# Performance work log

Hardware: AMD Instinct MI355X
Metric: run time of the kernel (lower is better)

## Reference

```python
import math
import jax, jax.numpy as jnp
import numpy as np

B, T, D, H, FACTOR = 8, 4096, 1024, 16, 5
DH = D // H


def setup_inputs() -> dict:
    key = jax.random.key(0)
    ks = jax.random.split(key, 7)
    u = max(1, min(int(FACTOR * math.log(T + 1)), T))  # = 41
    s = 1.0 / np.sqrt(D).astype(np.float32)
    x = jax.random.normal(ks[0], (B, T, D), jnp.float32)
    Wq = jax.random.normal(ks[1], (D, D), jnp.float32) * s
    Wk = jax.random.normal(ks[2], (D, D), jnp.float32) * s
    Wv = jax.random.normal(ks[3], (D, D), jnp.float32) * s
    Wo = jax.random.normal(ks[4], (D, D), jnp.float32) * s
    bo = jax.random.normal(ks[5], (D,), jnp.float32) * 0.01
    # unique indices, mirroring torch.randperm(T)[:u]
    idx = jax.random.permutation(ks[6], T)[:u].astype(jnp.int32)
    return {"x": x, "Wq": Wq, "Wk": Wk, "Wv": Wv, "Wo": Wo, "bo": bo, "idx": idx}


def reference(x, Wq, Wk, Wv, Wo, bo, idx):
    Bx, Tx, Dx = x.shape
    scale = 1.0 / np.sqrt(DH).astype(np.float32)

    def proj(W):  # torch Linear: x @ W.T, then split heads -> [B,H,T,Dh]
        return (x @ W.T).reshape(Bx, Tx, H, DH).transpose(0, 2, 1, 3)

    Q = proj(Wq)
    K = proj(Wk)
    V = proj(Wv)

    Qs = Q[:, :, idx, :]                                   # [B,H,u,Dh] gather
    scores = jnp.einsum('bhud,bhtd->bhut', Qs, K) * scale  # [B,H,u,T]
    attn = jax.nn.softmax(scores, axis=-1)
    ctx = jnp.einsum('bhut,bhtd->bhud', attn, V)           # [B,H,u,Dh]

    # mean over the u sampled positions fills non-sampled slots
    out = jnp.broadcast_to(ctx.mean(axis=2, keepdims=True), (Bx, H, Tx, DH))
    out = out.at[:, :, idx, :].set(ctx)                    # scatter ctx back

    y = out.transpose(0, 2, 1, 3).reshape(Bx, Tx, Dx)
    return y @ Wo.T + bo
```

## Files before the change

### kernel.cpp

```cpp
#include <hip/hip_runtime.h>
#include <hip/hip_bf16.h>

#define B_  8
#define T_  4096
#define D_  1024
#define H_  16
#define DH_ 64
#define NC_ 4

typedef __bf16 bf8 __attribute__((ext_vector_type(8)));
typedef float f32x4 __attribute__((ext_vector_type(4)));

__device__ __forceinline__ unsigned short f2bf_rn(float f) {
    unsigned u = __float_as_uint(f);
    unsigned r = (u + 0x7FFF + ((u >> 16) & 1)) >> 16;
    return (unsigned short)r;
}

__device__ __forceinline__ void async_load16(const void* gp, void* lp) {
    __builtin_amdgcn_global_load_lds(
        (const __attribute__((address_space(1))) unsigned*)(gp),
        (__attribute__((address_space(3))) unsigned*)(lp), 16, 0, 0);
}


__global__ void k_sel(const int* __restrict__ idx, int* __restrict__ sel, int U) {
    for (int t = threadIdx.x; t < T_; t += 256) sel[t] = 0;
    __syncthreads();
    if (threadIdx.x < U) sel[idx[threadIdx.x]] = threadIdx.x + 1;
}

__global__ void k_gather(const float* __restrict__ x, const int* __restrict__ idx,
                         float* __restrict__ xs, int U) {
    int bi = blockIdx.x;
    int b = bi / U, i = bi - b * U;
    int t = idx[i];
    const float4* src = (const float4*)(x + ((size_t)(b * T_ + t)) * D_);
    float4* dst = (float4*)(xs + (size_t)bi * D_);
    dst[threadIdx.x] = src[threadIdx.x];
}

__global__ void k_cvt_flat(const float* __restrict__ src, short* __restrict__ dst) {
    size_t i = ((size_t)blockIdx.x * 256 + threadIdx.x) * 8;
    float4 a = *(const float4*)(src + i);
    float4 b = *(const float4*)(src + i + 4);
    short4 s0, s1;
    s0.x = (short)f2bf_rn(a.x); s0.y = (short)f2bf_rn(a.y);
    s0.z = (short)f2bf_rn(a.z); s0.w = (short)f2bf_rn(a.w);
    s1.x = (short)f2bf_rn(b.x); s1.y = (short)f2bf_rn(b.y);
    s1.z = (short)f2bf_rn(b.z); s1.w = (short)f2bf_rn(b.w);
    *(short4*)(dst + i) = s0;
    *(short4*)(dst + i + 4) = s1;
}

__global__ void k_zpad(short* __restrict__ Qtb, int HU, int MP) {
    int bi = blockIdx.x;
    int npad = MP - HU;
    int b = bi / npad, r = bi - b * npad;
    short4 z = {0, 0, 0, 0};
    *(short4*)(Qtb + ((size_t)b * MP + HU + r) * D_ + threadIdx.x * 4) = z;
}

__global__ __launch_bounds__(256) void k_proj(const float* __restrict__ A,
                                              const float* __restrict__ W,
                                              const float* __restrict__ bias,
                                              float* __restrict__ C, int M) {
    __shared__ float As[32][64 + 4];
    __shared__ float Bs[32][64 + 4];
    int m0 = blockIdx.x * 64, n0 = blockIdx.y * 64;
    int tid = threadIdx.x;
    int lr = tid >> 3;
    int lc = (tid & 7) * 4;
    int ty = tid >> 4, tx = tid & 15;
    float acc[4][4] = {{0.f}};
    for (int k0 = 0; k0 < D_; k0 += 32) {
#pragma unroll
        for (int half = 0; half < 2; ++half) {
            int r = lr + half * 32;
            int gm = m0 + r;
            float4 v = make_float4(0.f, 0.f, 0.f, 0.f);
            if (gm < M) v = *(const float4*)(A + (size_t)gm * D_ + k0 + lc);
            As[lc + 0][r] = v.x; As[lc + 1][r] = v.y; As[lc + 2][r] = v.z; As[lc + 3][r] = v.w;
            int gn = n0 + r;
            float4 w = *(const float4*)(W + (size_t)gn * D_ + k0 + lc);
            Bs[lc + 0][r] = w.x; Bs[lc + 1][r] = w.y; Bs[lc + 2][r] = w.z; Bs[lc + 3][r] = w.w;
        }
        __syncthreads();
#pragma unroll
        for (int kk = 0; kk < 32; ++kk) {
            float4 a = *(const float4*)&As[kk][ty * 4];
            float4 bb = *(const float4*)&Bs[kk][tx * 4];
            acc[0][0] += a.x * bb.x; acc[0][1] += a.x * bb.y; acc[0][2] += a.x * bb.z; acc[0][3] += a.x * bb.w;
            acc[1][0] += a.y * bb.x; acc[1][1] += a.y * bb.y; acc[1][2] += a.y * bb.z; acc[1][3] += a.y * bb.w;
            acc[2][0] += a.z * bb.x; acc[2][1] += a.z * bb.y; acc[2][2] += a.z * bb.z; acc[2][3] += a.z * bb.w;
            acc[3][0] += a.w * bb.x; acc[3][1] += a.w * bb.y; acc[3][2] += a.w * bb.z; acc[3][3] += a.w * bb.w;
        }
        __syncthreads();
    }
#pragma unroll
    for (int i = 0; i < 4; ++i) {
        int gm = m0 + ty * 4 + i;
        if (gm < M) {
            int gn = n0 + tx * 4;
            float4 v = make_float4(acc[i][0], acc[i][1], acc[i][2], acc[i][3]);
            if (bias) {
                v.x += bias[gn + 0]; v.y += bias[gn + 1];
                v.z += bias[gn + 2]; v.w += bias[gn + 3];
            }
            *(float4*)(C + (size_t)gm * D_ + gn) = v;
        }
    }
}

__global__ __launch_bounds__(256) void k_qth(const float* __restrict__ Qs,
                                             const float* __restrict__ Wk,
                                             short* __restrict__ Qtb, int U, int MP) {
    __shared__ float As[32][64 + 4];
    __shared__ float Bs[32][64 + 4];
    int h = blockIdx.z;
    int m0 = blockIdx.x * 64, n0 = blockIdx.y * 64;
    int BU = B_ * U;
    int tid = threadIdx.x;
    int lr = tid >> 3, lc = (tid & 7) * 4;
    int ty = tid >> 4, tx = tid & 15;
    float acc[4][4] = {{0.f}};
    for (int k0 = 0; k0 < DH_; k0 += 32) {
#pragma unroll
        for (int half = 0; half < 2; ++half) {
            int r = lr + half * 32;
            int gm = m0 + r;
            float4 v = make_float4(0.f, 0.f, 0.f, 0.f);
            if (gm < BU) v = *(const float4*)(Qs + (size_t)gm * D_ + h * DH_ + k0 + lc);
            As[lc + 0][r] = v.x; As[lc + 1][r] = v.y; As[lc + 2][r] = v.z; As[lc + 3][r] = v.w;
            int kr = (tid >> 4) + half * 16;
            int nc = (tid & 15) * 4;
            float4 w = *(const float4*)(Wk + ((size_t)(h * DH_ + k0 + kr)) * D_ + n0 + nc);
            *(float4*)&Bs[kr][nc] = w;
        }
        __syncthreads();
#pragma unroll
        for (int kk = 0; kk < 32; ++kk) {
            float4 a = *(const float4*)&As[kk][ty * 4];
            float4 bb = *(const float4*)&Bs[kk][tx * 4];
            acc[0][0] += a.x * bb.x; acc[0][1] += a.x * bb.y; acc[0][2] += a.x * bb.z; acc[0][3] += a.x * bb.w;
            acc[1][0] += a.y * bb.x; acc[1][1] += a.y * bb.y; acc[1][2] += a.y * bb.z; acc[1][3] += a.y * bb.w;
            acc[2][0] += a.z * bb.x; acc[2][1] += a.z * bb.y; acc[2][2] += a.z * bb.z; acc[2][3] += a.z * bb.w;
            acc[3][0] += a.w * bb.x; acc[3][1] += a.w * bb.y; acc[3][2] += a.w * bb.z; acc[3][3] += a.w * bb.w;
        }
        __syncthreads();
    }
#pragma unroll
    for (int i = 0; i < 4; ++i) {
        int gm = m0 + ty * 4 + i;
        if (gm < BU) {
            int b = gm / U, ii = gm - b * U;
            short4 s;
            s.x = (short)f2bf_rn(0.125f * acc[i][0]);
            s.y = (short)f2bf_rn(0.125f * acc[i][1]);
            s.z = (short)f2bf_rn(0.125f * acc[i][2]);
            s.w = (short)f2bf_rn(0.125f * acc[i][3]);
            *(short4*)(Qtb + ((size_t)b * MP + h * U + ii) * D_ + n0 + tx * 4) = s;
        }
    }
}

__global__ __launch_bounds__(256) void k_scores_exp(const short* __restrict__ A,
                                                    const short* __restrict__ Bt,
                                                    short* __restrict__ attnb, int MP) {
    __shared__ short As[128 * 32];
    __shared__ short Bs[128 * 32];
    int g = blockIdx.x;
    int n8 = (g >> 3) & 3;
    int m = (g >> 5) % 6;
    int b = (g >> 5) / 6;
    int n = (g & 7) + 8 * n8;
    const int K = D_;
    const short* Ab = A + (size_t)b * MP * K;
    const short* Bb = Bt + (size_t)b * T_ * K;
    short* Cb = attnb + (size_t)b * MP * T_;
    int m0 = m * 128, n0 = n * 128;
    int tid = threadIdx.x;
    int lane = tid & 63, w = tid >> 6;
    int wr = w >> 1, wc = w & 1;

    f32x4 acc[4][4];
#pragma unroll
    for (int mi = 0; mi < 4; ++mi)
#pragma unroll
        for (int ni = 0; ni < 4; ++ni)
            acc[mi][ni] = (f32x4){0.f, 0.f, 0.f, 0.f};

    int arow = wr * 64 + (lane & 15);
    int brow = wc * 64 + (lane & 15);
    int koff = (lane >> 4) * 8;

    for (int kt = 0; kt < K; kt += 32) {
#pragma unroll
        for (int i = 0; i < 2; ++i) {
            int li = i * 256 + tid;
            int row = li >> 2, kc = (li & 3) << 3;
            async_load16(Ab + (size_t)(m0 + row) * K + kt + kc, As + li * 8);
            async_load16(Bb + (size_t)(n0 + row) * K + kt + kc, Bs + li * 8);
        }
        __syncthreads();
        bf8 af[4], bfr[4];
#pragma unroll
        for (int mi = 0; mi < 4; ++mi)
            af[mi] = *(const bf8*)(As + (arow + mi * 16) * 32 + koff);
#pragma unroll
        for (int ni = 0; ni < 4; ++ni)
            bfr[ni] = *(const bf8*)(Bs + (brow + ni * 16) * 32 + koff);
#pragma unroll
        for (int mi = 0; mi < 4; ++mi)
#pragma unroll
            for (int ni = 0; ni < 4; ++ni)
                acc[mi][ni] = __builtin_amdgcn_mfma_f32_16x16x32_bf16(af[mi], bfr[ni], acc[mi][ni], 0, 0, 0);
        __syncthreads();
    }

    int cr = (lane >> 4) * 4, cc = lane & 15;
#pragma unroll
    for (int mi = 0; mi < 4; ++mi)
#pragma unroll
        for (int ni = 0; ni < 4; ++ni) {
            int col = n0 + wc * 64 + ni * 16 + cc;
#pragma unroll
            for (int r = 0; r < 4; ++r) {
                float e = __expf(acc[mi][ni][r]);
                int grow = m0 + wr * 64 + mi * 16 + cr + r;
                Cb[(size_t)grow * T_ + col] = (short)f2bf_rn(e);
            }
        }
}

__global__ __launch_bounds__(256) void k_v(const short* __restrict__ xb,
                                           const short* __restrict__ Wvb,
                                           short* __restrict__ Vt) {
    __shared__ short smem[8192];
    short* As = smem;
    short* Bs = smem + 4096;
    int g = blockIdx.x;
    int mr = g & 7, n = (g >> 3) & 7, mq = g >> 6;
    int m = mq * 8 + mr;
    const int K = D_;
    const short* Ab = xb + (size_t)m * 128 * K;
    const short* Bb = Wvb + (size_t)n * 128 * K;
    int tid = threadIdx.x;
    int lane = tid & 63, w = tid >> 6;
    int wr = w >> 1, wc = w & 1;

    f32x4 acc[4][4];
#pragma unroll
    for (int mi = 0; mi < 4; ++mi)
#pragma unroll
        for (int ni = 0; ni < 4; ++ni)
            acc[mi][ni] = (f32x4){0.f, 0.f, 0.f, 0.f};

    int arow = wr * 64 + (lane & 15);
    int brow = wc * 64 + (lane & 15);
    int koff = (lane >> 4) * 8;

    for (int kt = 0; kt < K; kt += 32) {
#pragma unroll
        for (int i = 0; i < 2; ++i) {
            int li = i * 256 + tid;
            int row = li >> 2, kc = (li & 3) << 3;
            async_load16(Ab + (size_t)row * K + kt + kc, As + li * 8);
            async_load16(Bb + (size_t)row * K + kt + kc, Bs + li * 8);
        }
        __syncthreads();
        bf8 af[4], bfr[4];
#pragma unroll
        for (int mi = 0; mi < 4; ++mi)
            af[mi] = *(const bf8*)(As + (arow + mi * 16) * 32 + koff);
#pragma unroll
        for (int ni = 0; ni < 4; ++ni)
            bfr[ni] = *(const bf8*)(Bs + (brow + ni * 16) * 32 + koff);
#pragma unroll
        for (int mi = 0; mi < 4; ++mi)
#pragma unroll
            for (int ni = 0; ni < 4; ++ni)
                acc[mi][ni] = __builtin_amdgcn_mfma_f32_16x16x32_bf16(af[mi], bfr[ni], acc[mi][ni], 0, 0, 0);
        __syncthreads();
    }

    int b = m >> 5;
    int tG0 = (m & 31) * 128 + wr * 64;
    int h = n * 2 + wc;
    short* ep = smem + w * 2048;
    const int PITCH = 72;
    int quad = lane >> 4;
#pragma unroll
    for (int ni = 0; ni < 4; ++ni) {
#pragma unroll
        for (int mi = 0; mi < 4; ++mi) {
            int t = mi * 16 + quad * 4;
            int dh = lane & 15;
#pragma unroll
            for (int r = 0; r < 4; ++r)
                ep[dh * PITCH + t + r] = (short)f2bf_rn(acc[mi][ni][r]);
        }
        __syncthreads();
#pragma unroll
        for (int it = 0; it < 2; ++it) {
            int dhl = it * 8 + (lane >> 3);
            int seg = lane & 7;
            bf8 v = *(const bf8*)(ep + dhl * PITCH + seg * 8);
            int dh = ni * 16 + dhl;
            *(bf8*)(Vt + ((size_t)(b * H_ + h) * DH_ + dh) * T_ + tG0 + seg * 8) = v;
        }
        __syncthreads();
    }
}

__global__ __launch_bounds__(256) void k_pv(const short* __restrict__ attnb,
                                            const short* __restrict__ Vt,
                                            float* __restrict__ Op,
                                            float* __restrict__ rsp,
                                            int U, int MP) {
    __shared__ short vt[64 * 136];
    int gid = blockIdx.x;
    int c = gid & (NC_ - 1);
    int bh = gid >> 2;
    int h = bh & (H_ - 1);
    int b = bh >> 4;
    int tid = threadIdx.x;
    int lane = tid & 63, w = tid >> 6;
    int quad = lane >> 4;
    const short* Arow = attnb + ((size_t)b * MP + h * U) * T_;
    const short* Vrow = Vt + (size_t)bh * DH_ * T_;

    f32x4 O[3];
#pragma unroll
    for (int mi = 0; mi < 3; ++mi) O[mi] = (f32x4){0.f, 0.f, 0.f, 0.f};
    float rs[3] = {0.f, 0.f, 0.f};

    for (int tt = 0; tt < (T_ / NC_) / 128; ++tt) {
        int t0 = c * (T_ / NC_) + tt * 128;
#pragma unroll
        for (int it = 0; it < 4; ++it) {
            int idx = it * 256 + tid;
            int dh = idx >> 4, seg = idx & 15;
            bf8 v = *(const bf8*)(Vrow + (size_t)dh * T_ + t0 + seg * 8);
            *(bf8*)(vt + dh * 136 + seg * 8) = v;
        }
        __syncthreads();
        bf8 af[3][4];
#pragma unroll
        for (int mi = 0; mi < 3; ++mi)
#pragma unroll
            for (int kf = 0; kf < 4; ++kf)
                af[mi][kf] = *(const bf8*)(Arow + (size_t)(mi * 16 + (lane & 15)) * T_ + t0 + kf * 32 + quad * 8);
        if (w == 0) {
#pragma unroll
            for (int mi = 0; mi < 3; ++mi)
#pragma unroll
                for (int kf = 0; kf < 4; ++kf)
#pragma unroll
                    for (int j = 0; j < 8; ++j) rs[mi] += (float)af[mi][kf][j];
        }
#pragma unroll
        for (int kf = 0; kf < 4; ++kf) {
            bf8 bfr = *(const bf8*)(vt + (w * 16 + (lane & 15)) * 136 + kf * 32 + quad * 8);
#pragma unroll
            for (int mi = 0; mi < 3; ++mi)
                O[mi] = __builtin_amdgcn_mfma_f32_16x16x32_bf16(af[mi][kf], bfr, O[mi], 0, 0, 0);
        }
        __syncthreads();
    }
#pragma unroll
    for (int mi = 0; mi < 3; ++mi)
#pragma unroll
        for (int r = 0; r < 4; ++r)
            Op[((size_t)gid * 48 + mi * 16 + quad * 4 + r) * DH_ + w * 16 + (lane & 15)] = O[mi][r];
    if (w == 0) {
#pragma unroll
        for (int mi = 0; mi < 3; ++mi) {
            rs[mi] += __shfl_xor(rs[mi], 16);
            rs[mi] += __shfl_xor(rs[mi], 32);
            if (quad == 0) rsp[(size_t)gid * 48 + mi * 16 + lane] = rs[mi];
        }
    }
}

__global__ __launch_bounds__(256) void k_rows2(const float* __restrict__ Op,
                                               const float* __restrict__ rsp,
                                               float* __restrict__ R, int U) {
    __shared__ float inv[48];
    __shared__ float msum[4][64];
    int bh = blockIdx.x;
    int b = bh >> 4, h = bh & (H_ - 1);
    int tid = threadIdx.x;
    if (tid < 48) {
        float s = 0.f;
        for (int cc = 0; cc < NC_; ++cc) s += rsp[(size_t)(bh * NC_ + cc) * 48 + tid];
        inv[tid] = 1.f / s;
    }
    __syncthreads();
    int dh = tid & 63, ig = tid >> 6;
    float acc = 0.f;
    for (int p = 0; p < 11; ++p) {
        int i = p * 4 + ig;
        if (i < U) {
            float o = 0.f;
            for (int cc = 0; cc < NC_; ++cc)
                o += Op[((size_t)(bh * NC_ + cc) * 48 + i) * DH_ + dh];
            float v = o * inv[i];
            R[((size_t)b * (U + 1) + 1 + i) * D_ + h * DH_ + dh] = v;
            acc += v;
        }
    }
    msum[ig][dh] = acc;
    __syncthreads();
    if (ig == 0)
        R[((size_t)b * (U + 1)) * D_ + h * DH_ + dh] =
            (msum[0][dh] + msum[1][dh] + msum[2][dh] + msum[3][dh]) / (float)U;
}

__global__ __launch_bounds__(256) void k_fill(const float* __restrict__ Yr,
                                              const int* __restrict__ sel,
                                              float* __restrict__ y, int U) {
    int blk = blockIdx.x;
    int b = blk >> 12, t = blk & (T_ - 1);
    int j = sel[t];
    const float4* src = (const float4*)(Yr + ((size_t)b * (U + 1) + j) * D_);
    float4* dst = (float4*)(y + (size_t)blk * D_);
    dst[threadIdx.x] = src[threadIdx.x];
}

extern "C" void kernel_launch(void* const* d_in, const int* in_sizes, int n_in,
                              void* d_out, int out_size, void* d_ws, size_t ws_size,
                              hipStream_t stream) {
    const float* x  = (const float*)d_in[0];
    const float* Wq = (const float*)d_in[1];
    const float* Wk = (const float*)d_in[2];
    const float* Wv = (const float*)d_in[3];
    const float* Wo = (const float*)d_in[4];
    const float* bo = (const float*)d_in[5];
    const int*  idx = (const int*)d_in[6];
    int U = in_sizes[6];
    int HU = H_ * U;
    int MP = ((HU + 127) / 128) * 128;

    char* w = (char*)d_ws;
    auto alloc = [&](size_t bytes) { char* p = w; w += (bytes + 255) & ~(size_t)255; return p; };

    float* xs    = (float*)alloc((size_t)B_ * U * D_ * 4);
    float* Qs    = (float*)alloc((size_t)B_ * U * D_ * 4);
    short* Qtb   = (short*)alloc((size_t)B_ * MP * D_ * 2);
    short* xb    = (short*)alloc((size_t)B_ * T_ * D_ * 2);
    short* Wvb   = (short*)alloc((size_t)D_ * D_ * 2);
    short* attnb = (short*)alloc((size_t)B_ * MP * T_ * 2);
    short* Vtb   = (short*)alloc((size_t)B_ * D_ * T_ * 2);
    float* Opb   = (float*)alloc((size_t)B_ * H_ * NC_ * 48 * DH_ * 4);
    float* rspb  = (float*)alloc((size_t)B_ * H_ * NC_ * 48 * 4);
    float* R     = (float*)alloc((size_t)B_ * (U + 1) * D_ * 4);
    float* Yr    = (float*)alloc((size_t)B_ * (U + 1) * D_ * 4);
    int*   sel   = (int*)alloc((size_t)T_ * 4);

    k_sel<<<dim3(1), dim3(256), 0, stream>>>(idx, sel, U);
    k_gather<<<dim3(B_ * U), dim3(256), 0, stream>>>(x, idx, xs, U);
    k_proj<<<dim3((B_ * U + 63) / 64, D_ / 64), dim3(256), 0, stream>>>(xs, Wq, nullptr, Qs, B_ * U);
    k_cvt_flat<<<dim3((size_t)B_ * T_ * D_ / 2048), dim3(256), 0, stream>>>(x, xb);
    k_cvt_flat<<<dim3((size_t)D_ * D_ / 2048), dim3(256), 0, stream>>>(Wv, Wvb);
    k_zpad<<<dim3(B_ * (MP - HU)), dim3(256), 0, stream>>>(Qtb, HU, MP);
    k_qth<<<dim3((B_ * U + 63) / 64, D_ / 64, H_), dim3(256), 0, stream>>>(Qs, Wk, Qtb, U, MP);
    k_scores_exp<<<dim3(8 * 4 * 6 * B_), dim3(256), 0, stream>>>(Qtb, xb, attnb, MP);
    k_v<<<dim3(2048), dim3(256), 0, stream>>>(xb, Wvb, Vtb);
    k_pv<<<dim3(B_ * H_ * NC_), dim3(256), 0, stream>>>(attnb, Vtb, Opb, rspb, U, MP);
    k_rows2<<<dim3(B_ * H_), dim3(256), 0, stream>>>(Opb, rspb, R, U);
    k_proj<<<dim3((B_ * (U + 1) + 63) / 64, D_ / 64), dim3(256), 0, stream>>>(R, Wo, bo, Yr, B_ * (U + 1));
    k_fill<<<dim3(B_ * T_), dim3(256), 0, stream>>>(Yr, sel, (float*)d_out, U);
}
```

Before: 589.4 us.

## Merge prep kernels, fuse gather into Q projection, co-launch V and scores GEMMs

Folds the sel, bf16 conversion and zero-pad kernels into one prep launch, and fuses the row gather into the Q projection so the gathered copy disappears. The V projection and the scores+exp GEMM now run as two block ranges of a single launch, so they can overlap on the GPU. The scores epilogue swaps MFMA operand order to write short4 vectors, and the V transpose epilogue uses vector LDS writes with a new pitch and drops barriers. This cuts launch count and tail idle time, at the cost of a combined kernel whose register and LDS use is set by the heavier branch.

Result: no change. 596.5 us (+1.2%).

```diff
diff --git a/kernel.cpp b/kernel.cpp
--- a/kernel.cpp
+++ b/kernel.cpp
@@ -23,42 +23,88 @@
         (__attribute__((address_space(3))) unsigned*)(lp), 16, 0, 0);
 }
 
-
-__global__ void k_sel(const int* __restrict__ idx, int* __restrict__ sel, int U) {
-    for (int t = threadIdx.x; t < T_; t += 256) sel[t] = 0;
+__global__ void k_prep(const float* __restrict__ x, short* __restrict__ xb,
+                       const float* __restrict__ Wv, short* __restrict__ Wvb,
+                       short* __restrict__ Qtb, const int* __restrict__ idx,
+                       int* __restrict__ sel, int U, int HU, int MP, int nzp) {
+    int g = blockIdx.x;
+    int tid = threadIdx.x;
+    if (g < 16896) {
+        const float* src = (g < 16384) ? x : Wv;
+        short* dst = (g < 16384) ? xb : Wvb;
+        size_t gg = (g < 16384) ? g : (g - 16384);
+        size_t i = (gg * 256 + tid) * 8;
+        float4 a = *(const float4*)(src + i);
+        float4 b = *(const float4*)(src + i + 4);
+        short4 s0, s1;
+        s0.x = (short)f2bf_rn(a.x); s0.y = (short)f2bf_rn(a.y);
+        s0.z = (short)f2bf_rn(a.z); s0.w = (short)f2bf_rn(a.w);
+        s1.x = (short)f2bf_rn(b.x); s1.y = (short)f2bf_rn(b.y);
+        s1.z = (short)f2bf_rn(b.z); s1.w = (short)f2bf_rn(b.w);
+        *(short4*)(dst + i) = s0;
+        *(short4*)(dst + i + 4) = s1;
+    } else if (g < 16896 + nzp) {
+        int bi = g - 16896;
+        int npad = MP - HU;
+        int b = bi / npad, r = bi - b * npad;
+        short4 z = {0, 0, 0, 0};
+        *(short4*)(Qtb + ((size_t)b * MP + HU + r) * D_ + tid * 4) = z;
+    } else {
+        for (int t = tid; t < T_; t += 256) sel[t] = 0;
+        __syncthreads();
+        if (tid < U) sel[idx[tid]] = tid + 1;
+    }
+}
+
+__global__ __launch_bounds__(256) void k_projg(const float* __restrict__ x,
+                                               const int* __restrict__ idx,
+                                               const float* __restrict__ W,
+                                               float* __restrict__ C, int U) {
+    __shared__ float As[32][64 + 4];
+    __shared__ float Bs[32][64 + 4];
+    __shared__ int sidx[64];
+    int M = B_ * U;
+    if (threadIdx.x < U) sidx[threadIdx.x] = idx[threadIdx.x];
     __syncthreads();
-    if (threadIdx.x < U) sel[idx[threadIdx.x]] = threadIdx.x + 1;
-}
-
-__global__ void k_gather(const float* __restrict__ x, const int* __restrict__ idx,
-                         float* __restrict__ xs, int U) {
-    int bi = blockIdx.x;
-    int b = bi / U, i = bi - b * U;
-    int t = idx[i];
-    const float4* src = (const float4*)(x + ((size_t)(b * T_ + t)) * D_);
-    float4* dst = (float4*)(xs + (size_t)bi * D_);
-    dst[threadIdx.x] = src[threadIdx.x];
-}
-
-__global__ void k_cvt_flat(const float* __restrict__ src, short* __restrict__ dst) {
-    size_t i = ((size_t)blockIdx.x * 256 + threadIdx.x) * 8;
-    float4 a = *(const float4*)(src + i);
-    float4 b = *(const float4*)(src + i + 4);
-    short4 s0, s1;
-    s0.x = (short)f2bf_rn(a.x); s0.y = (short)f2bf_rn(a.y);
-    s0.z = (short)f2bf_rn(a.z); s0.w = (short)f2bf_rn(a.w);
-    s1.x = (short)f2bf_rn(b.x); s1.y = (short)f2bf_rn(b.y);
-    s1.z = (short)f2bf_rn(b.z); s1.w = (short)f2bf_rn(b.w);
-    *(short4*)(dst + i) = s0;
-    *(short4*)(dst + i + 4) = s1;
-}
-
-__global__ void k_zpad(short* __restrict__ Qtb, int HU, int MP) {
-    int bi = blockIdx.x;
-    int npad = MP - HU;
-    int b = bi / npad, r = bi - b * npad;
-    short4 z = {0, 0, 0, 0};
-    *(short4*)(Qtb + ((size_t)b * MP + HU + r) * D_ + threadIdx.x * 4) = z;
+    int m0 = blockIdx.x * 64, n0 = blockIdx.y * 64;
+    int tid = threadIdx.x;
+    int lr = tid >> 3, lc = (tid & 7) * 4;
+    int ty = tid >> 4, tx = tid & 15;
+    float acc[4][4] = {{0.f}};
+    for (int k0 = 0; k0 < D_; k0 += 32) {
+#pragma unroll
+        for (int half = 0; half < 2; ++half) {
+            int r = lr + half * 32;
+            int gm = m0 + r;
+            float4 v = make_float4(0.f, 0.f, 0.f, 0.f);
+            if (gm < M) {
+                int b = gm / U, i = gm - b * U;
+                v = *(const float4*)(x + ((size_t)(b * T_ + sidx[i])) * D_ + k0 + lc);
+            }
+            As[lc + 0][r] = v.x; As[lc + 1][r] = v.y; As[lc + 2][r] = v.z; As[lc + 3][r] = v.w;
+            int gn = n0 + r;
+            float4 w = *(const float4*)(W + (size_t)gn * D_ + k0 + lc);
+            Bs[lc + 0][r] = w.x; Bs[lc + 1][r] = w.y; Bs[lc + 2][r] = w.z; Bs[lc + 3][r] = w.w;
+        }
+        __syncthreads();
+#pragma unroll
+        for (int kk = 0; kk < 32; ++kk) {
+            float4 a = *(const float4*)&As[kk][ty * 4];
+            float4 bb = *(const float4*)&Bs[kk][tx * 4];
+            acc[0][0] += a.x * bb.x; acc[0][1] += a.x * bb.y; acc[0][2] += a.x * bb.z; acc[0][3] += a.x * bb.w;
+            acc[1][0] += a.y * bb.x; acc[1][1] += a.y * bb.y; acc[1][2] += a.y * bb.z; acc[1][3] += a.y * bb.w;
+            acc[2][0] += a.z * bb.x; acc[2][1] += a.z * bb.y; acc[2][2] += a.z * bb.z; acc[2][3] += a.z * bb.w;
+            acc[3][0] += a.w * bb.x; acc[3][1] += a.w * bb.y; acc[3][2] += a.w * bb.z; acc[3][3] += a.w * bb.w;
+        }
+        __syncthreads();
+    }
+#pragma unroll
+    for (int i = 0; i < 4; ++i) {
+        int gm = m0 + ty * 4 + i;
+        if (gm < M)
+            *(float4*)(C + (size_t)gm * D_ + n0 + tx * 4) =
+                make_float4(acc[i][0], acc[i][1], acc[i][2], acc[i][3]);
+    }
 }
 
 __global__ __launch_bounds__(256) void k_proj(const float* __restrict__ A,
@@ -69,8 +115,7 @@
     __shared__ float Bs[32][64 + 4];
     int m0 = blockIdx.x * 64, n0 = blockIdx.y * 64;
     int tid = threadIdx.x;
-    int lr = tid >> 3;
-    int lc = (tid & 7) * 4;
+    int lr = tid >> 3, lc = (tid & 7) * 4;
     int ty = tid >> 4, tx = tid & 15;
     float acc[4][4] = {{0.f}};
     for (int k0 = 0; k0 < D_; k0 += 32) {
@@ -164,90 +209,20 @@
     }
 }
 
-__global__ __launch_bounds__(256) void k_scores_exp(const short* __restrict__ A,
-                                                    const short* __restrict__ Bt,
-                                                    short* __restrict__ attnb, int MP) {
-    __shared__ short As[128 * 32];
-    __shared__ short Bs[128 * 32];
-    int g = blockIdx.x;
-    int n8 = (g >> 3) & 3;
-    int m = (g >> 5) % 6;
-    int b = (g >> 5) / 6;
-    int n = (g & 7) + 8 * n8;
-    const int K = D_;
-    const short* Ab = A + (size_t)b * MP * K;
-    const short* Bb = Bt + (size_t)b * T_ * K;
-    short* Cb = attnb + (size_t)b * MP * T_;
-    int m0 = m * 128, n0 = n * 128;
-    int tid = threadIdx.x;
-    int lane = tid & 63, w = tid >> 6;
-    int wr = w >> 1, wc = w & 1;
-
-    f32x4 acc[4][4];
-#pragma unroll
-    for (int mi = 0; mi < 4; ++mi)
-#pragma unroll
-        for (int ni = 0; ni < 4; ++ni)
-            acc[mi][ni] = (f32x4){0.f, 0.f, 0.f, 0.f};
-
-    int arow = wr * 64 + (lane & 15);
-    int brow = wc * 64 + (lane & 15);
-    int koff = (lane >> 4) * 8;
-
-    for (int kt = 0; kt < K; kt += 32) {
-#pragma unroll
-        for (int i = 0; i < 2; ++i) {
-            int li = i * 256 + tid;
-            int row = li >> 2, kc = (li & 3) << 3;
-            async_load16(Ab + (size_t)(m0 + row) * K + kt + kc, As + li * 8);
-            async_load16(Bb + (size_t)(n0 + row) * K + kt + kc, Bs + li * 8);
-        }
-        __syncthreads();
-        bf8 af[4], bfr[4];
-#pragma unroll
-        for (int mi = 0; mi < 4; ++mi)
-            af[mi] = *(const bf8*)(As + (arow + mi * 16) * 32 + koff);
-#pragma unroll
-        for (int ni = 0; ni < 4; ++ni)
-            bfr[ni] = *(const bf8*)(Bs + (brow + ni * 16) * 32 + koff);
-#pragma unroll
-        for (int mi = 0; mi < 4; ++mi)
-#pragma unroll
-            for (int ni = 0; ni < 4; ++ni)
-                acc[mi][ni] = __builtin_amdgcn_mfma_f32_16x16x32_bf16(af[mi], bfr[ni], acc[mi][ni], 0, 0, 0);
-        __syncthreads();
-    }
-
-    int cr = (lane >> 4) * 4, cc = lane & 15;
-#pragma unroll
-    for (int mi = 0; mi < 4; ++mi)
-#pragma unroll
-        for (int ni = 0; ni < 4; ++ni) {
-            int col = n0 + wc * 64 + ni * 16 + cc;
-#pragma unroll
-            for (int r = 0; r < 4; ++r) {
-                float e = __expf(acc[mi][ni][r]);
-                int grow = m0 + wr * 64 + mi * 16 + cr + r;
-                Cb[(size_t)grow * T_ + col] = (short)f2bf_rn(e);
-            }
-        }
-}
-
-__global__ __launch_bounds__(256) void k_v(const short* __restrict__ xb,
-                                           const short* __restrict__ Wvb,
-                                           short* __restrict__ Vt) {
+__global__ __launch_bounds__(256) void k_scores_v(const short* __restrict__ Qtb,
+                                                  const short* __restrict__ xb,
+                                                  const short* __restrict__ Wvb,
+                                                  short* __restrict__ attnb,
+                                                  short* __restrict__ Vt, int MP) {
     __shared__ short smem[8192];
     short* As = smem;
     short* Bs = smem + 4096;
     int g = blockIdx.x;
-    int mr = g & 7, n = (g >> 3) & 7, mq = g >> 6;
-    int m = mq * 8 + mr;
-    const int K = D_;
-    const short* Ab = xb + (size_t)m * 128 * K;
-    const short* Bb = Wvb + (size_t)n * 128 * K;
     int tid = threadIdx.x;
     int lane = tid & 63, w = tid >> 6;
     int wr = w >> 1, wc = w & 1;
+    int quad = lane >> 4, l15 = lane & 15;
+    const int K = D_;
 
     f32x4 acc[4][4];
 #pragma unroll
@@ -256,60 +231,109 @@
         for (int ni = 0; ni < 4; ++ni)
             acc[mi][ni] = (f32x4){0.f, 0.f, 0.f, 0.f};
 
-    int arow = wr * 64 + (lane & 15);
-    int brow = wc * 64 + (lane & 15);
-    int koff = (lane >> 4) * 8;
-
-    for (int kt = 0; kt < K; kt += 32) {
-#pragma unroll
-        for (int i = 0; i < 2; ++i) {
-            int li = i * 256 + tid;
-            int row = li >> 2, kc = (li & 3) << 3;
-            async_load16(Ab + (size_t)row * K + kt + kc, As + li * 8);
-            async_load16(Bb + (size_t)row * K + kt + kc, Bs + li * 8);
-        }
-        __syncthreads();
-        bf8 af[4], bfr[4];
-#pragma unroll
-        for (int mi = 0; mi < 4; ++mi)
-            af[mi] = *(const bf8*)(As + (arow + mi * 16) * 32 + koff);
+    int arow = wr * 64 + l15;
+    int brow = wc * 64 + l15;
+    int koff = quad * 8;
+
+    if (g < 2048) {
+        int mr = g & 7, n = (g >> 3) & 7, mq = g >> 6;
+        int m = mq * 8 + mr;
+        const short* Ab = xb + (size_t)m * 128 * K;
+        const short* Bb = Wvb + (size_t)n * 128 * K;
+        for (int kt = 0; kt < K; kt += 32) {
+#pragma unroll
+            for (int i = 0; i < 2; ++i) {
+                int li = i * 256 + tid;
+                int row = li >> 2, kc = (li & 3) << 3;
+                async_load16(Ab + (size_t)row * K + kt + kc, As + li * 8);
+                async_load16(Bb + (size_t)row * K + kt + kc, Bs + li * 8);
+            }
+            __syncthreads();
+            bf8 af[4], bfr[4];
+#pragma unroll
+            for (int mi = 0; mi < 4; ++mi)
+                af[mi] = *(const bf8*)(As + (arow + mi * 16) * 32 + koff);
+#pragma unroll
+            for (int ni = 0; ni < 4; ++ni)
+                bfr[ni] = *(const bf8*)(Bs + (brow + ni * 16) * 32 + koff);
+#pragma unroll
+            for (int mi = 0; mi < 4; ++mi)
+#pragma unroll
+                for (int ni = 0; ni < 4; ++ni)
+                    acc[mi][ni] = __builtin_amdgcn_mfma_f32_16x16x32_bf16(af[mi], bfr[ni], acc[mi][ni], 0, 0, 0);
+            __syncthreads();
+        }
+        int b = m >> 5;
+        int tG0 = (m & 31) * 128 + wr * 64;
+        int h = n * 2 + wc;
+        short* ep = smem + w * 2048;
+        const int PITCH = 80;
+#pragma unroll
+        for (int ni = 0; ni < 4; ++ni) {
+#pragma unroll
+            for (int mi = 0; mi < 4; ++mi) {
+                short4 s;
+                s.x = (short)f2bf_rn(acc[mi][ni][0]);
+                s.y = (short)f2bf_rn(acc[mi][ni][1]);
+                s.z = (short)f2bf_rn(acc[mi][ni][2]);
+                s.w = (short)f2bf_rn(acc[mi][ni][3]);
+                *(short4*)(ep + l15 * PITCH + mi * 16 + quad * 4) = s;
+            }
+#pragma unroll
+            for (int it = 0; it < 2; ++it) {
+                int dhl = it * 8 + (lane >> 3);
+                int seg = lane & 7;
+                bf8 v = *(const bf8*)(ep + dhl * PITCH + seg * 8);
+                int dh = ni * 16 + dhl;
+                *(bf8*)(Vt + ((size_t)(b * H_ + h) * DH_ + dh) * T_ + tG0 + seg * 8) = v;
+            }
+        }
+    } else {
+        int gs = g - 2048;
+        int n8 = (gs >> 3) & 3;
+        int m = (gs >> 5) % 6;
+        int b = (gs >> 5) / 6;
+        int n = (gs & 7) + 8 * n8;
+        const short* Ab = Qtb + (size_t)b * MP * K;
+        const short* Bb = xb + (size_t)b * T_ * K;
+        short* Cb = attnb + (size_t)b * MP * T_;
+        int m0 = m * 128, n0 = n * 128;
+        for (int kt = 0; kt < K; kt += 32) {
+#pragma unroll
+            for (int i = 0; i < 2; ++i) {
+                int li = i * 256 + tid;
+                int row = li >> 2, kc = (li & 3) << 3;
+                async_load16(Ab + (size_t)(m0 + row) * K + kt + kc, As + li * 8);
+                async_load16(Bb + (size_t)(n0 + row) * K + kt + kc, Bs + li * 8);
+            }
+            __syncthreads();
+            bf8 af[4], bfr[4];
+#pragma unroll
+            for (int mi = 0; mi < 4; ++mi)
+                af[mi] = *(const bf8*)(As + (arow + mi * 16) * 32 + koff);
+#pragma unroll
+            for (int ni = 0; ni < 4; ++ni)
+                bfr[ni] = *(const bf8*)(Bs + (brow + ni * 16) * 32 + koff);
+#pragma unroll
+            for (int ni = 0; ni < 4; ++ni)
+#pragma unroll
+                for (int mi = 0; mi < 4; ++mi)
+                    acc[ni][mi] = __builtin_amdgcn_mfma_f32_16x16x32_bf16(bfr[ni], af[mi], acc[ni][mi], 0, 0, 0);
+            __syncthreads();
+        }
 #pragma unroll
         for (int ni = 0; ni < 4; ++ni)
-            bfr[ni] = *(const bf8*)(Bs + (brow + ni * 16) * 32 + koff);
-#pragma unroll
-        for (int mi = 0; mi < 4; ++mi)
-#pragma unroll
-            for (int ni = 0; ni < 4; ++ni)
-                acc[mi][ni] = __builtin_amdgcn_mfma_f32_16x16x32_bf16(af[mi], bfr[ni], acc[mi][ni], 0, 0, 0);
-        __syncthreads();
-    }
-
-    int b = m >> 5;
-    int tG0 = (m & 31) * 128 + wr * 64;
-    int h = n * 2 + wc;
-    short* ep = smem + w * 2048;
-    const int PITCH = 72;
-    int quad = lane >> 4;
-#pragma unroll
-    for (int ni = 0; ni < 4; ++ni) {
-#pragma unroll
-        for (int mi = 0; mi < 4; ++mi) {
-            int t = mi * 16 + quad * 4;
-            int dh = lane & 15;
-#pragma unroll
-            for (int r = 0; r < 4; ++r)
-                ep[dh * PITCH + t + r] = (short)f2bf_rn(acc[mi][ni][r]);
-        }
-        __syncthreads();
-#pragma unroll
-        for (int it = 0; it < 2; ++it) {
-            int dhl = it * 8 + (lane >> 3);
-            int seg = lane & 7;
-            bf8 v = *(const bf8*)(ep + dhl * PITCH + seg * 8);
-            int dh = ni * 16 + dhl;
-            *(bf8*)(Vt + ((size_t)(b * H_ + h) * DH_ + dh) * T_ + tG0 + seg * 8) = v;
-        }
-        __syncthreads();
+#pragma unroll
+            for (int mi = 0; mi < 4; ++mi) {
+                int grow = m0 + wr * 64 + mi * 16 + l15;
+                int col = n0 + wc * 64 + ni * 16 + quad * 4;
+                short4 s;
+                s.x = (short)f2bf_rn(__expf(acc[ni][mi][0]));
+                s.y = (short)f2bf_rn(__expf(acc[ni][mi][1]));
+                s.z = (short)f2bf_rn(__expf(acc[ni][mi][2]));
+                s.w = (short)f2bf_rn(__expf(acc[ni][mi][3]));
+                *(short4*)(Cb + (size_t)grow * T_ + col) = s;
+            }
     }
 }
 
@@ -441,11 +465,11 @@
     int U = in_sizes[6];
     int HU = H_ * U;
     int MP = ((HU + 127) / 128) * 128;
+    int nzp = B_ * (MP - HU);
 
     char* w = (char*)d_ws;
     auto alloc = [&](size_t bytes) { char* p = w; w += (bytes + 255) & ~(size_t)255; return p; };
 
-    float* xs    = (float*)alloc((size_t)B_ * U * D_ * 4);
     float* Qs    = (float*)alloc((size_t)B_ * U * D_ * 4);
     short* Qtb   = (short*)alloc((size_t)B_ * MP * D_ * 2);
     short* xb    = (short*)alloc((size_t)B_ * T_ * D_ * 2);
@@ -458,15 +482,10 @@
     float* Yr    = (float*)alloc((size_t)B_ * (U + 1) * D_ * 4);
     int*   sel   = (int*)alloc((size_t)T_ * 4);
 
-    k_sel<<<dim3(1), dim3(256), 0, stream>>>(idx, sel, U);
-    k_gather<<<dim3(B_ * U), dim3(256), 0, stream>>>(x, idx, xs, U);
-    k_proj<<<dim3((B_ * U + 63) / 64, D_ / 64), dim3(256), 0, stream>>>(xs, Wq, nullptr, Qs, B_ * U);
-    k_cvt_flat<<<dim3((size_t)B_ * T_ * D_ / 2048), dim3(256), 0, stream>>>(x, xb);
-    k_cvt_flat<<<dim3((size_t)D_ * D_ / 2048), dim3(256), 0, stream>>>(Wv, Wvb);
-    k_zpad<<<dim3(B_ * (MP - HU)), dim3(256), 0, stream>>>(Qtb, HU, MP);
+    k_prep<<<dim3(16896 + nzp + 1), dim3(256), 0, stream>>>(x, xb, Wv, Wvb, Qtb, idx, sel, U, HU, MP, nzp);
+    k_projg<<<dim3((B_ * U + 63) / 64, D_ / 64), dim3(256), 0, stream>>>(x, idx, Wq, Qs, U);
     k_qth<<<dim3((B_ * U + 63) / 64, D_ / 64, H_), dim3(256), 0, stream>>>(Qs, Wk, Qtb, U, MP);
-    k_scores_exp<<<dim3(8 * 4 * 6 * B_), dim3(256), 0, stream>>>(Qtb, xb, attnb, MP);
-    k_v<<<dim3(2048), dim3(256), 0, stream>>>(xb, Wvb, Vtb);
+    k_scores_v<<<dim3(2048 + 8 * 4 * 6 * B_), dim3(256), 0, stream>>>(Qtb, xb, Wvb, attnb, Vtb, MP);
     k_pv<<<dim3(B_ * H_ * NC_), dim3(256), 0, stream>>>(attnb, Vtb, Opb, rspb, U, MP);
     k_rows2<<<dim3(B_ * H_), dim3(256), 0, stream>>>(Opb, rspb, R, U);
     k_proj<<<dim3((B_ * (U + 1) + 63) / 64, D_ / 64), dim3(256), 0, stream>>>(R, Wo, bo, Yr, B_ * (U + 1));
```
